# Kernel tuning notes

Measured on AMD Instinct MI355X. Metric: run time of the kernel, lower is better.

## Reference

```python
import jax, jax.numpy as jnp
import numpy as np

MARGIN = 0.2
NEG_INF = -1e9  # safe stand-in for -inf when masking the max


def setup_inputs() -> dict:
    key = jax.random.key(0)
    k1, k2, k3 = jax.random.split(key, 3)
    B, D = 8192, 256
    p = jax.random.normal(k1, (B, D), dtype=jnp.float32)
    # module docstring says projections are normalized
    projections = p / jnp.linalg.norm(p, axis=1, keepdims=True)
    affordance_ids = jax.random.randint(k2, (B,), 0, 36, dtype=jnp.int64)
    instance_ids = jax.random.randint(k3, (B,), 0, 2048, dtype=jnp.int64)
    return {
        "projections": projections,
        "affordance_ids": affordance_ids,
        "instance_ids": instance_ids,
    }


def reference(projections, affordance_ids, instance_ids):
    # (B, B) cosine similarities
    sim = jnp.matmul(projections, projections.T)

    aff_eq = affordance_ids[:, None] == affordance_ids[None, :]
    inst_eq = instance_ids[:, None] == instance_ids[None, :]
    pos_mask = aff_eq & ~inst_eq          # same affordance, different instance
    neg_mask = ~aff_eq                    # different affordance

    # per-row hard negative: max similarity over negatives
    hard_neg = jnp.max(jnp.where(neg_mask, sim, NEG_INF), axis=1)  # (B,)

    # rows contribute only if they have >=1 positive AND >=1 negative
    valid_row = pos_mask.any(axis=1) & neg_mask.any(axis=1)        # (B,)
    pair_mask = pos_mask & valid_row[:, None]                      # (B, B)

    # margin loss for every (anchor i, positive j) pair
    losses = jnp.maximum(hard_neg[:, None] - sim + MARGIN, 0.0)

    total = jnp.sum(jnp.where(pair_mask, losses, 0.0))
    num_pairs = jnp.sum(pair_mask)
    return jnp.where(num_pairs > 0, total / num_pairs, 0.0)
```

## Files before the change

kernel.cpp:

```cpp
#include <hip/hip_runtime.h>

#define NB 8192
#define ND 256
#define NCLS 64
#define LOSS_MARGIN 0.2f
#define NEG_INF_F (-1e9f)
#define LMAXT 3
#define NBLK_LOSS (NCLS * LMAXT * LMAXT)
#define NTILE_T 2080

typedef __attribute__((ext_vector_type(8))) __bf16 bf16x8;
typedef __attribute__((ext_vector_type(4))) float f32x4;

__device__ __forceinline__ unsigned short f2bf(float f) {
  unsigned u = __float_as_uint(f);
  unsigned r = (u + 0x7fffu + ((u >> 16) & 1u)) >> 16;
  return (unsigned short)r;
}

__device__ __forceinline__ void gl_lds16(const void* gsrc, void* ldst) {
  __builtin_amdgcn_global_load_lds(
      (const __attribute__((address_space(1))) void*)gsrc,
      (__attribute__((address_space(3))) void*)ldst, 16, 0, 0);
}

__global__ __launch_bounds__(1024) void build_idx_fused(const int* __restrict__ aff,
                                                        int* __restrict__ class_start,
                                                        int* __restrict__ class_idx) {
  const int c = blockIdx.x;
  const int t = threadIdx.x;
  const int lane = t & 63, wave = t >> 6;
  __shared__ int wtot[16];
  __shared__ int s_off;

  int lt = 0;
  for (int i = t; i < NB; i += 1024) lt += (aff[i] < c) ? 1 : 0;
  for (int off = 32; off; off >>= 1) lt += __shfl_down(lt, off);
  if (lane == 0) wtot[wave] = lt;
  __syncthreads();
  int base = 0;
  for (int w = 0; w < 16; ++w) base += wtot[w];
  if (t == 0) {
    class_start[c] = base;
    if (c == 0) class_start[NCLS] = NB;
  }
  __syncthreads();
  if (t == 0) s_off = 0;
  __syncthreads();

  for (int pass = 0; pass < NB / 1024; ++pass) {
    const int i = pass * 1024 + t;
    const bool m = (aff[i] == c);
    const unsigned long long mask = __ballot(m);
    if (lane == 0) wtot[wave] = __popcll(mask);
    __syncthreads();
    const int off = s_off;
    int prefix = 0;
    for (int w = 0; w < wave; ++w) prefix += wtot[w];
    if (m)
      class_idx[base + off + prefix +
                __popcll(mask & ((1ull << lane) - 1ull))] = i;
    __syncthreads();
    if (t == 0) {
      int tot = 0;
      for (int w = 0; w < 16; ++w) tot += wtot[w];
      s_off = off + tot;
    }
    __syncthreads();
  }
}

__global__ __launch_bounds__(256) void gather_convert(const float* __restrict__ P,
                                                      const int* __restrict__ aff,
                                                      const int* __restrict__ inst,
                                                      const int* __restrict__ class_idx,
                                                      unsigned short* __restrict__ Psort,
                                                      int* __restrict__ affSort,
                                                      int* __restrict__ instSort) {
  const int t = threadIdx.x;
  const int sr = blockIdx.x * 8 + (t >> 5);
  const int c = t & 31;
  const int src = class_idx[sr];
  const float4* ps = (const float4*)(P + (size_t)src * ND);
  ushort4* pd = (ushort4*)(Psort + (size_t)sr * ND);
#pragma unroll
  for (int q = 0; q < 2; ++q) {
    float4 v = ps[c + q * 32];
    ushort4 h;
    h.x = f2bf(v.x); h.y = f2bf(v.y); h.z = f2bf(v.z); h.w = f2bf(v.w);
    pd[c + q * 32] = h;
  }
  if (c == 0) {
    affSort[sr] = aff[src];
    instSort[sr] = inst[src];
  }
}

__global__ __launch_bounds__(256, 4) void simmax_mfma(const unsigned short* __restrict__ Psort,
                                                      const int* __restrict__ affSort,
                                                      float* __restrict__ part) {
  int wg = blockIdx.x;
  wg = (wg & 7) * (NTILE_T / 8) + (wg >> 3);
  int bi = (int)((129.0f - sqrtf(129.0f * 129.0f - 8.0f * (float)wg)) * 0.5f);
  while (bi * 64 - bi * (bi - 1) / 2 > wg) --bi;
  while ((bi + 1) * 64 - (bi + 1) * bi / 2 <= wg) ++bi;
  const int bj = bi + (wg - (bi * 64 - bi * (bi - 1) / 2));

  __shared__ __align__(16) unsigned short smemu[16384];
  float* rowmax_s = (float*)&smemu[0];
  float* colmax_s = (float*)&smemu[512];

  const int t = threadIdx.x;
  const int lane = t & 63;
  const int wave = t >> 6;
  const int r0 = bi * 128, c0 = bj * 128;

  const bool needMask = (affSort[c0] <= affSort[r0 + 127]);

  const int wr = (wave >> 1) * 64;
  const int wc = (wave & 1) * 64;

  f32x4 acc[4][4];
#pragma unroll
  for (int m = 0; m < 4; ++m)
#pragma unroll
    for (int n = 0; n < 4; ++n) acc[m][n] = (f32x4){0.f, 0.f, 0.f, 0.f};

  const int ci0 = t, ci1 = 256 + t;
  const int kg0 = ci0 >> 7, rw0 = ci0 & 127;
  const int kg1 = ci1 >> 7, rw1 = ci1 & 127;

#define STAGE_SIM(B, KC)                                                      \
  do {                                                                        \
    gl_lds16(Psort + (size_t)(r0 + rw0) * ND + (KC) + kg0 * 8,                \
             &smemu[(B) * 4096 + ci0 * 8]);                                   \
    gl_lds16(Psort + (size_t)(c0 + rw0) * ND + (KC) + kg0 * 8,                \
             &smemu[8192 + (B) * 4096 + ci0 * 8]);                            \
    gl_lds16(Psort + (size_t)(r0 + rw1) * ND + (KC) + kg1 * 8,                \
             &smemu[(B) * 4096 + ci1 * 8]);                                   \
    gl_lds16(Psort + (size_t)(c0 + rw1) * ND + (KC) + kg1 * 8,                \
             &smemu[8192 + (B) * 4096 + ci1 * 8]);                            \
  } while (0)

  STAGE_SIM(0, 0);
  asm volatile("s_waitcnt vmcnt(0) lgkmcnt(0)" ::: "memory");
  __builtin_amdgcn_s_barrier();
  __builtin_amdgcn_sched_barrier(0);

  int cur = 0;
#pragma unroll 1
  for (int s = 0; s < 8; ++s) {
    if (s < 7) STAGE_SIM(cur ^ 1, (s + 1) * 32);
    const int kg = lane >> 4, lr = lane & 15;
    bf16x8 a[4], b[4];
#pragma unroll
    for (int m = 0; m < 4; ++m)
      a[m] = *(const bf16x8*)&smemu[cur * 4096 + (kg * 128 + wr + m * 16 + lr) * 8];
#pragma unroll
    for (int n = 0; n < 4; ++n)
      b[n] = *(const bf16x8*)&smemu[8192 + cur * 4096 + (kg * 128 + wc + n * 16 + lr) * 8];
#pragma unroll
    for (int m = 0; m < 4; ++m)
#pragma unroll
      for (int n = 0; n < 4; ++n)
        acc[m][n] = __builtin_amdgcn_mfma_f32_16x16x32_bf16(a[m], b[n], acc[m][n], 0, 0, 0);
    __builtin_amdgcn_sched_barrier(0);
    if (s < 7) {
      asm volatile("s_waitcnt vmcnt(0)" ::: "memory");
      __builtin_amdgcn_s_barrier();
      __builtin_amdgcn_sched_barrier(0);
    }
    cur ^= 1;
  }

  if (needMask) {
#pragma unroll
    for (int m = 0; m < 4; ++m) {
#pragma unroll
      for (int r = 0; r < 4; ++r) {
        const int lrow = wr + m * 16 + (lane >> 4) * 4 + r;
        const int ai = affSort[r0 + lrow];
        float rmax = NEG_INF_F;
#pragma unroll
        for (int n = 0; n < 4; ++n) {
          const int lcol = wc + n * 16 + (lane & 15);
          if (affSort[c0 + lcol] != ai) rmax = fmaxf(rmax, acc[m][n][r]);
        }
        rmax = fmaxf(rmax, __shfl_xor(rmax, 1));
        rmax = fmaxf(rmax, __shfl_xor(rmax, 2));
        rmax = fmaxf(rmax, __shfl_xor(rmax, 4));
        rmax = fmaxf(rmax, __shfl_xor(rmax, 8));
        if ((lane & 15) == 0) rowmax_s[lrow * 2 + (wc >> 6)] = rmax;
      }
    }
    if (bi != bj) {
#pragma unroll
      for (int n = 0; n < 4; ++n) {
        const int lcol = wc + n * 16 + (lane & 15);
        const int aj = affSort[c0 + lcol];
        float cmax = NEG_INF_F;
#pragma unroll
        for (int m = 0; m < 4; ++m) {
          const int lrb = wr + m * 16 + (lane >> 4) * 4;
#pragma unroll
          for (int r = 0; r < 4; ++r)
            if (affSort[r0 + lrb + r] != aj) cmax = fmaxf(cmax, acc[m][n][r]);
        }
        cmax = fmaxf(cmax, __shfl_xor(cmax, 16));
        cmax = fmaxf(cmax, __shfl_xor(cmax, 32));
        if (lane < 16) colmax_s[lcol * 2 + (wr >> 6)] = cmax;
      }
    }
  } else {
#pragma unroll
    for (int m = 0; m < 4; ++m) {
#pragma unroll
      for (int r = 0; r < 4; ++r) {
        float rmax = fmaxf(fmaxf(acc[m][0][r], acc[m][1][r]),
                           fmaxf(acc[m][2][r], acc[m][3][r]));
        rmax = fmaxf(rmax, __shfl_xor(rmax, 1));
        rmax = fmaxf(rmax, __shfl_xor(rmax, 2));
        rmax = fmaxf(rmax, __shfl_xor(rmax, 4));
        rmax = fmaxf(rmax, __shfl_xor(rmax, 8));
        if ((lane & 15) == 0)
          rowmax_s[(wr + m * 16 + (lane >> 4) * 4 + r) * 2 + (wc >> 6)] = rmax;
      }
    }
#pragma unroll
    for (int n = 0; n < 4; ++n) {
      float cmax = NEG_INF_F;
#pragma unroll
      for (int m = 0; m < 4; ++m)
#pragma unroll
        for (int r = 0; r < 4; ++r) cmax = fmaxf(cmax, acc[m][n][r]);
      cmax = fmaxf(cmax, __shfl_xor(cmax, 16));
      cmax = fmaxf(cmax, __shfl_xor(cmax, 32));
      if (lane < 16) colmax_s[(wc + n * 16 + (lane & 15)) * 2 + (wr >> 6)] = cmax;
    }
  }
  __syncthreads();
  if (t < 128) {
    part[(size_t)bj * NB + (r0 + t)] = fmaxf(rowmax_s[t * 2], rowmax_s[t * 2 + 1]);
  } else if (bi != bj) {
    const int cc = t - 128;
    part[(size_t)bi * NB + (c0 + cc)] = fmaxf(colmax_s[cc * 2], colmax_s[cc * 2 + 1]);
  }
#undef STAGE_SIM
}

__global__ __launch_bounds__(256, 4) void loss_mfma(const unsigned short* __restrict__ Psort,
                                                    const int* __restrict__ class_start,
                                                    const int* __restrict__ instSort,
                                                    const float* __restrict__ part,
                                                    float* __restrict__ bsum,
                                                    int* __restrict__ bcnt) {
  const int c = blockIdx.z;
  const int ti = blockIdx.x, tj = blockIdx.y;
  const int bid = (c * LMAXT + ti) * LMAXT + tj;
  const int t = threadIdx.x;
  const int base = class_start[c];
  const int cnt = class_start[c + 1] - base;
  const int nt = (cnt + 127) >> 7;
  if (ti >= nt || tj >= nt || cnt >= NB) {
    if (t == 0) { bsum[bid] = 0.f; bcnt[bid] = 0; }
    return;
  }

  __shared__ __align__(16) unsigned short At[2][4096];
  __shared__ __align__(16) unsigned short Bt[2][4096];
  __shared__ int instI[128], instJ[128];
  __shared__ float hnI[128];

  const int lane = t & 63;
  const int wave = t >> 6;

  if (t < 128) {
    int ri = ti * 128 + t;
    int gi = base + (ri < cnt ? ri : 0);
    instI[t] = instSort[gi];
    float m = NEG_INF_F;
#pragma unroll 16
    for (int q = 0; q < 64; ++q) m = fmaxf(m, part[(size_t)q * NB + gi]);
    hnI[t] = m;
  } else {
    int tt = t - 128;
    int rj = tj * 128 + tt;
    int gj = base + (rj < cnt ? rj : 0);
    instJ[tt] = instSort[gj];
  }

  const int wr = (wave >> 1) * 64;
  const int wc = (wave & 1) * 64;

  f32x4 acc[4][4];
#pragma unroll
  for (int m = 0; m < 4; ++m)
#pragma unroll
    for (int n = 0; n < 4; ++n) acc[m][n] = (f32x4){0.f, 0.f, 0.f, 0.f};

  const int ci0 = t, ci1 = 256 + t;
  const int kg0 = ci0 >> 7, rw0 = ci0 & 127;
  const int kg1 = ci1 >> 7, rw1 = ci1 & 127;
  const int ra0 = base + (ti * 128 + rw0 < cnt ? ti * 128 + rw0 : 0);
  const int ra1 = base + (ti * 128 + rw1 < cnt ? ti * 128 + rw1 : 0);
  const int rb0 = base + (tj * 128 + rw0 < cnt ? tj * 128 + rw0 : 0);
  const int rb1 = base + (tj * 128 + rw1 < cnt ? tj * 128 + rw1 : 0);

#define STAGE_LOSS(B, KC)                                               \
  do {                                                                  \
    gl_lds16(Psort + (size_t)ra0 * ND + (KC) + kg0 * 8, &At[B][ci0 * 8]); \
    gl_lds16(Psort + (size_t)rb0 * ND + (KC) + kg0 * 8, &Bt[B][ci0 * 8]); \
    gl_lds16(Psort + (size_t)ra1 * ND + (KC) + kg1 * 8, &At[B][ci1 * 8]); \
    gl_lds16(Psort + (size_t)rb1 * ND + (KC) + kg1 * 8, &Bt[B][ci1 * 8]); \
  } while (0)

  STAGE_LOSS(0, 0);
  asm volatile("s_waitcnt vmcnt(0) lgkmcnt(0)" ::: "memory");
  __builtin_amdgcn_s_barrier();
  __builtin_amdgcn_sched_barrier(0);

  int cur = 0;
#pragma unroll 1
  for (int s = 0; s < 8; ++s) {
    if (s < 7) STAGE_LOSS(cur ^ 1, (s + 1) * 32);
    const int kg = lane >> 4, lr = lane & 15;
    bf16x8 a[4], b[4];
#pragma unroll
    for (int m = 0; m < 4; ++m)
      a[m] = *(const bf16x8*)&At[cur][(kg * 128 + wr + m * 16 + lr) * 8];
#pragma unroll
    for (int n = 0; n < 4; ++n)
      b[n] = *(const bf16x8*)&Bt[cur][(kg * 128 + wc + n * 16 + lr) * 8];
#pragma unroll
    for (int m = 0; m < 4; ++m)
#pragma unroll
      for (int n = 0; n < 4; ++n)
        acc[m][n] = __builtin_amdgcn_mfma_f32_16x16x32_bf16(a[m], b[n], acc[m][n], 0, 0, 0);
    __builtin_amdgcn_sched_barrier(0);
    if (s < 7) {
      asm volatile("s_waitcnt vmcnt(0)" ::: "memory");
      __builtin_amdgcn_s_barrier();
      __builtin_amdgcn_sched_barrier(0);
    }
    cur ^= 1;
  }

  float lsum = 0.f;
  int lcnt = 0;
#pragma unroll
  for (int m = 0; m < 4; ++m) {
#pragma unroll
    for (int r = 0; r < 4; ++r) {
      const int lrow = wr + m * 16 + (lane >> 4) * 4 + r;
      const int ri = ti * 128 + lrow;
      if (ri >= cnt) continue;
      const float hnv = hnI[lrow];
      const int ii = instI[lrow];
#pragma unroll
      for (int n = 0; n < 4; ++n) {
        const int lcol = wc + n * 16 + (lane & 15);
        const int rj = tj * 128 + lcol;
        if (rj < cnt && instJ[lcol] != ii) {
          lsum += fmaxf(hnv - acc[m][n][r] + LOSS_MARGIN, 0.f);
          lcnt += 1;
        }
      }
    }
  }

  for (int off = 32; off; off >>= 1) {
    lsum += __shfl_down(lsum, off);
    lcnt += __shfl_down(lcnt, off);
  }
  __shared__ float wsum[4];
  __shared__ int wcnt[4];
  if (lane == 0) { wsum[wave] = lsum; wcnt[wave] = lcnt; }
  __syncthreads();
  if (t == 0) {
    bsum[bid] = wsum[0] + wsum[1] + wsum[2] + wsum[3];
    bcnt[bid] = wcnt[0] + wcnt[1] + wcnt[2] + wcnt[3];
  }
#undef STAGE_LOSS
}

__global__ __launch_bounds__(256) void finalize_kernel(const float* __restrict__ bsum,
                                                       const int* __restrict__ bcnt,
                                                       float* __restrict__ out) {
  const int t = threadIdx.x;
  float s = 0.f;
  int n = 0;
  for (int i = t; i < NBLK_LOSS; i += 256) { s += bsum[i]; n += bcnt[i]; }
  for (int off = 32; off; off >>= 1) {
    s += __shfl_down(s, off);
    n += __shfl_down(n, off);
  }
  __shared__ float wsum[4];
  __shared__ int wcnt[4];
  if ((t & 63) == 0) { wsum[t >> 6] = s; wcnt[t >> 6] = n; }
  __syncthreads();
  if (t == 0) {
    const float S = wsum[0] + wsum[1] + wsum[2] + wsum[3];
    const int N = wcnt[0] + wcnt[1] + wcnt[2] + wcnt[3];
    out[0] = (N > 0) ? (S / (float)N) : 0.0f;
  }
}

extern "C" void kernel_launch(void* const* d_in, const int* in_sizes, int n_in,
                              void* d_out, int out_size, void* d_ws, size_t ws_size,
                              hipStream_t stream) {
  const float* P = (const float*)d_in[0];
  const int* aff = (const int*)d_in[1];
  const int* inst = (const int*)d_in[2];
  float* out = (float*)d_out;

  unsigned short* Psort = (unsigned short*)d_ws;
  float* part = (float*)((char*)d_ws + (size_t)NB * ND * 2);
  int* ibase = (int*)((char*)part + (size_t)64 * NB * 4);
  int* class_start = ibase;
  int* class_idx   = ibase + NCLS + 1;
  int* affSort     = ibase + NCLS + 1 + NB;
  int* instSort    = ibase + NCLS + 1 + 2 * NB;
  float* bsum = (float*)(ibase + NCLS + 1 + 3 * NB);
  int* bcnt   = ibase + NCLS + 1 + 3 * NB + NBLK_LOSS;

  build_idx_fused<<<NCLS, 1024, 0, stream>>>(aff, class_start, class_idx);
  gather_convert<<<NB / 8, 256, 0, stream>>>(P, aff, inst, class_idx, Psort,
                                             affSort, instSort);
  simmax_mfma<<<NTILE_T, 256, 0, stream>>>(Psort, affSort, part);
  loss_mfma<<<dim3(LMAXT, LMAXT, NCLS), 256, 0, stream>>>(Psort, class_start, instSort,
                                                          part, bsum, bcnt);
  finalize_kernel<<<1, 256, 0, stream>>>(bsum, bcnt, out);
}
```

Before: 93.04 us.

## Rewrite class index build with register scan and add separate hard-negative reduce kernel

The per-class index build now runs with 256 threads, each loading 32 contiguous labels into registers. Output positions come from a wave-level shuffle scan, which replaces the 8-pass ballot loop and its many block barriers. The per-row hard-negative max over the 64 partial results moves out of loss_mfma into a small hn_reduce kernel, so each loss block reads one value per row instead of 64 strided loads. In simmax, the column affinity loads are hoisted into registers. The cost is one extra kernel launch and a workspace layout shift.

```diff
diff --git a/kernel.cpp b/kernel.cpp
--- a/kernel.cpp
+++ b/kernel.cpp
@@ -7,6 +7,7 @@
 #define NEG_INF_F (-1e9f)
 #define LMAXT 3
 #define NBLK_LOSS (NCLS * LMAXT * LMAXT)
+#define NT 64
 #define NTILE_T 2080
 
 typedef __attribute__((ext_vector_type(8))) __bf16 bf16x8;
@@ -24,50 +25,48 @@
       (__attribute__((address_space(3))) void*)ldst, 16, 0, 0);
 }
 
-__global__ __launch_bounds__(1024) void build_idx_fused(const int* __restrict__ aff,
-                                                        int* __restrict__ class_start,
-                                                        int* __restrict__ class_idx) {
+__global__ __launch_bounds__(256) void build_idx(const int* __restrict__ aff,
+                                                 int* __restrict__ class_start,
+                                                 int* __restrict__ class_idx) {
   const int c = blockIdx.x;
   const int t = threadIdx.x;
   const int lane = t & 63, wave = t >> 6;
-  __shared__ int wtot[16];
-  __shared__ int s_off;
-
-  int lt = 0;
-  for (int i = t; i < NB; i += 1024) lt += (aff[i] < c) ? 1 : 0;
-  for (int off = 32; off; off >>= 1) lt += __shfl_down(lt, off);
-  if (lane == 0) wtot[wave] = lt;
+  __shared__ int wtotLT[4];
+  __shared__ int wtotEQ[4];
+
+  int a[32];
+#pragma unroll
+  for (int k = 0; k < 32; ++k) a[k] = aff[t * 32 + k];
+  int ltc = 0, meq = 0;
+#pragma unroll
+  for (int k = 0; k < 32; ++k) {
+    ltc += (a[k] < c) ? 1 : 0;
+    meq += (a[k] == c) ? 1 : 0;
+  }
+
+  int sc = meq;
+  for (int d = 1; d < 64; d <<= 1) {
+    int n = __shfl_up(sc, d);
+    if (lane >= d) sc += n;
+  }
+  int ltr = ltc;
+  for (int off = 32; off; off >>= 1) ltr += __shfl_down(ltr, off);
+  if (lane == 63) wtotEQ[wave] = sc;
+  if (lane == 0) wtotLT[wave] = ltr;
   __syncthreads();
-  int base = 0;
-  for (int w = 0; w < 16; ++w) base += wtot[w];
+
+  int base = wtotLT[0] + wtotLT[1] + wtotLT[2] + wtotLT[3];
+  int wpre = 0;
+  for (int w = 0; w < wave; ++w) wpre += wtotEQ[w];
+  int p = base + wpre + (sc - meq);
+
   if (t == 0) {
     class_start[c] = base;
     if (c == 0) class_start[NCLS] = NB;
   }
-  __syncthreads();
-  if (t == 0) s_off = 0;
-  __syncthreads();
-
-  for (int pass = 0; pass < NB / 1024; ++pass) {
-    const int i = pass * 1024 + t;
-    const bool m = (aff[i] == c);
-    const unsigned long long mask = __ballot(m);
-    if (lane == 0) wtot[wave] = __popcll(mask);
-    __syncthreads();
-    const int off = s_off;
-    int prefix = 0;
-    for (int w = 0; w < wave; ++w) prefix += wtot[w];
-    if (m)
-      class_idx[base + off + prefix +
-                __popcll(mask & ((1ull << lane) - 1ull))] = i;
-    __syncthreads();
-    if (t == 0) {
-      int tot = 0;
-      for (int w = 0; w < 16; ++w) tot += wtot[w];
-      s_off = off + tot;
-    }
-    __syncthreads();
-  }
+#pragma unroll
+  for (int k = 0; k < 32; ++k)
+    if (a[k] == c) class_idx[p++] = t * 32 + k;
 }
 
 __global__ __launch_bounds__(256) void gather_convert(const float* __restrict__ P,
@@ -174,6 +173,9 @@
   }
 
   if (needMask) {
+    int aj[4];
+#pragma unroll
+    for (int n = 0; n < 4; ++n) aj[n] = affSort[c0 + wc + n * 16 + (lane & 15)];
 #pragma unroll
     for (int m = 0; m < 4; ++m) {
 #pragma unroll
@@ -182,10 +184,8 @@
         const int ai = affSort[r0 + lrow];
         float rmax = NEG_INF_F;
 #pragma unroll
-        for (int n = 0; n < 4; ++n) {
-          const int lcol = wc + n * 16 + (lane & 15);
-          if (affSort[c0 + lcol] != ai) rmax = fmaxf(rmax, acc[m][n][r]);
-        }
+        for (int n = 0; n < 4; ++n)
+          if (aj[n] != ai) rmax = fmaxf(rmax, acc[m][n][r]);
         rmax = fmaxf(rmax, __shfl_xor(rmax, 1));
         rmax = fmaxf(rmax, __shfl_xor(rmax, 2));
         rmax = fmaxf(rmax, __shfl_xor(rmax, 4));
@@ -197,14 +197,13 @@
 #pragma unroll
       for (int n = 0; n < 4; ++n) {
         const int lcol = wc + n * 16 + (lane & 15);
-        const int aj = affSort[c0 + lcol];
         float cmax = NEG_INF_F;
 #pragma unroll
         for (int m = 0; m < 4; ++m) {
           const int lrb = wr + m * 16 + (lane >> 4) * 4;
 #pragma unroll
           for (int r = 0; r < 4; ++r)
-            if (affSort[r0 + lrb + r] != aj) cmax = fmaxf(cmax, acc[m][n][r]);
+            if (affSort[r0 + lrb + r] != aj[n]) cmax = fmaxf(cmax, acc[m][n][r]);
         }
         cmax = fmaxf(cmax, __shfl_xor(cmax, 16));
         cmax = fmaxf(cmax, __shfl_xor(cmax, 32));
@@ -248,10 +247,19 @@
 #undef STAGE_SIM
 }
 
+__global__ __launch_bounds__(256) void hn_reduce(const float* __restrict__ part,
+                                                 float* __restrict__ hn) {
+  const int i = blockIdx.x * 256 + threadIdx.x;
+  float m = NEG_INF_F;
+#pragma unroll 16
+  for (int q = 0; q < NT; ++q) m = fmaxf(m, part[(size_t)q * NB + i]);
+  hn[i] = m;
+}
+
 __global__ __launch_bounds__(256, 4) void loss_mfma(const unsigned short* __restrict__ Psort,
                                                     const int* __restrict__ class_start,
                                                     const int* __restrict__ instSort,
-                                                    const float* __restrict__ part,
+                                                    const float* __restrict__ hn,
                                                     float* __restrict__ bsum,
                                                     int* __restrict__ bcnt) {
   const int c = blockIdx.z;
@@ -278,10 +286,7 @@
     int ri = ti * 128 + t;
     int gi = base + (ri < cnt ? ri : 0);
     instI[t] = instSort[gi];
-    float m = NEG_INF_F;
-#pragma unroll 16
-    for (int q = 0; q < 64; ++q) m = fmaxf(m, part[(size_t)q * NB + gi]);
-    hnI[t] = m;
+    hnI[t] = hn[gi];
   } else {
     int tt = t - 128;
     int rj = tj * 128 + tt;
@@ -415,19 +420,21 @@
 
   unsigned short* Psort = (unsigned short*)d_ws;
   float* part = (float*)((char*)d_ws + (size_t)NB * ND * 2);
-  int* ibase = (int*)((char*)part + (size_t)64 * NB * 4);
-  int* class_start = ibase;
-  int* class_idx   = ibase + NCLS + 1;
-  int* affSort     = ibase + NCLS + 1 + NB;
-  int* instSort    = ibase + NCLS + 1 + 2 * NB;
-  float* bsum = (float*)(ibase + NCLS + 1 + 3 * NB);
-  int* bcnt   = ibase + NCLS + 1 + 3 * NB + NBLK_LOSS;
-
-  build_idx_fused<<<NCLS, 1024, 0, stream>>>(aff, class_start, class_idx);
+  int* ibase = (int*)((char*)part + (size_t)NT * NB * 4);
+  float* hn        = (float*)ibase;
+  int* class_start = ibase + NB;
+  int* class_idx   = ibase + NB + NCLS + 1;
+  int* affSort     = ibase + 2 * NB + NCLS + 1;
+  int* instSort    = ibase + 3 * NB + NCLS + 1;
+  float* bsum = (float*)(ibase + 4 * NB + NCLS + 1);
+  int* bcnt   = ibase + 4 * NB + NCLS + 1 + NBLK_LOSS;
+
+  build_idx<<<NCLS, 256, 0, stream>>>(aff, class_start, class_idx);
   gather_convert<<<NB / 8, 256, 0, stream>>>(P, aff, inst, class_idx, Psort,
                                              affSort, instSort);
   simmax_mfma<<<NTILE_T, 256, 0, stream>>>(Psort, affSort, part);
+  hn_reduce<<<NB / 256, 256, 0, stream>>>(part, hn);
   loss_mfma<<<dim3(LMAXT, LMAXT, NCLS), 256, 0, stream>>>(Psort, class_start, instSort,
-                                                          part, bsum, bcnt);
+                                                          hn, bsum, bcnt);
   finalize_kernel<<<1, 256, 0, stream>>>(bsum, bcnt, out);
 }
```

Result: faster. 89.48 us (median of 2 runs) (-3.8%).
